# Kernel tuning notes

Hardware: AMD Instinct MI355X
Metric: run time of the kernel (lower is better)

The kernel has to match this reference:

```python
import jax, jax.numpy as jnp
import numpy as np

B, S, D_MODEL, N_HEADS, HEAD_DIM = 4, 2048, 1024, 16, 64
NEG = -1e9


def apply_rope_real(x, cos_f, sin_f):
    # x: [B, H, S, D]; cos_f/sin_f: [S, D//2] broadcast over B, H
    x_even = x[..., ::2]
    x_odd = x[..., 1::2]
    out_even = x_even * cos_f - x_odd * sin_f
    out_odd = x_even * sin_f + x_odd * cos_f
    return jnp.stack([out_even, out_odd], axis=-1).reshape(x.shape)


def setup_inputs() -> dict:
    key = jax.random.key(0)
    ks = jax.random.split(key, 8)
    x = jax.random.normal(ks[0], (B, S, D_MODEL), dtype=jnp.float32)
    # RoPE tables: theta_i = 10000^{-2i/d}, angles = pos * theta
    inv_freq = 1.0 / (10000.0 ** (jnp.arange(0, HEAD_DIM, 2, dtype=jnp.float32) / HEAD_DIM))
    angles = jnp.arange(S, dtype=jnp.float32)[:, None] * inv_freq[None, :]  # [S, D/2]
    cos_freqs = jnp.cos(angles)
    sin_freqs = jnp.sin(angles)
    causal_mask = jnp.where(jnp.tril(jnp.ones((S, S), dtype=bool)), 0.0, NEG).astype(jnp.float32)
    scale = 0.02
    w_q = jax.random.normal(ks[1], (D_MODEL, D_MODEL), dtype=jnp.float32) * scale
    w_k = jax.random.normal(ks[2], (D_MODEL, D_MODEL), dtype=jnp.float32) * scale
    w_v = jax.random.normal(ks[3], (D_MODEL, D_MODEL), dtype=jnp.float32) * scale
    w_o = jax.random.normal(ks[4], (D_MODEL, D_MODEL), dtype=jnp.float32) * scale
    return {"x": x, "cos_freqs": cos_freqs, "sin_freqs": sin_freqs,
            "causal_mask": causal_mask, "w_q": w_q, "w_k": w_k, "w_v": w_v, "w_o": w_o}


def reference(x, cos_freqs, sin_freqs, causal_mask, w_q, w_k, w_v, w_o):
    batch, seq_len, _ = x.shape
    scale = 1.0 / jnp.sqrt(jnp.float32(HEAD_DIM))
    # torch Linear: y = x @ W.T
    def proj(w):
        return (x @ w.T).reshape(batch, seq_len, N_HEADS, HEAD_DIM).transpose(0, 2, 1, 3)
    q = apply_rope_real(proj(w_q), cos_freqs, sin_freqs)
    k = apply_rope_real(proj(w_k), cos_freqs, sin_freqs)
    v = proj(w_v)
    attn = jnp.einsum('bhqd,bhkd->bhqk', q, k) * scale + causal_mask
    attn = jax.nn.softmax(attn, axis=-1)
    out = jnp.einsum('bhqk,bhkd->bhqd', attn, v)
    out = out.transpose(0, 2, 1, 3).reshape(batch, seq_len, -1)
    return out @ w_o.T
```

## Files before the change

kernel.cpp:

```cpp
#include <hip/hip_runtime.h>
#include <stdint.h>

#define B_  4
#define S_  2048
#define DM_ 1024
#define NH_ 16
#define HD_ 64

typedef unsigned short ushort_t;
typedef __bf16 bf16x8 __attribute__((ext_vector_type(8)));
typedef float  floatx4 __attribute__((ext_vector_type(4)));
typedef float  floatx16 __attribute__((ext_vector_type(16)));

__device__ __forceinline__ float bf2f(ushort_t u) {
    union { unsigned int i; float f; } v; v.i = ((unsigned int)u) << 16; return v.f;
}
__device__ __forceinline__ ushort_t f2bf(float f) {
    union { float f; unsigned int i; } v; v.f = f;
    unsigned int x = v.i;
    return (ushort_t)((x + 0x7fffu + ((x >> 16) & 1u)) >> 16);
}
__device__ __forceinline__ unsigned int pack_bf16_trunc(float lo, float hi) {
    union { float f; unsigned int u; } a, b;
    a.f = lo; b.f = hi;
    return __builtin_amdgcn_perm(b.u, a.u, 0x07060302u);
}

__global__ __launch_bounds__(256) void cvt_all_kernel(
    const float* __restrict__ x,  const float* __restrict__ wq,
    const float* __restrict__ wk, const float* __restrict__ wv,
    const float* __restrict__ wo,
    ushort_t* __restrict__ xb,  ushort_t* __restrict__ wqb,
    ushort_t* __restrict__ wkb, ushort_t* __restrict__ wvb,
    ushort_t* __restrict__ wob)
{
    const int blk = blockIdx.x;
    const float* src; ushort_t* dst; int off;
    if (blk < 8192)       { src = x;  dst = xb;  off = blk; }
    else if (blk < 9216)  { src = wq; dst = wqb; off = blk - 8192; }
    else if (blk < 10240) { src = wk; dst = wkb; off = blk - 9216; }
    else if (blk < 11264) { src = wv; dst = wvb; off = blk - 10240; }
    else                  { src = wo; dst = wob; off = blk - 11264; }
    const int i = off * 256 + threadIdx.x;
    float4 v = ((const float4*)src)[i];
    ushort4 o; o.x = f2bf(v.x); o.y = f2bf(v.y); o.z = f2bf(v.z); o.w = f2bf(v.w);
    ((ushort4*)dst)[i] = o;
}

__global__ __launch_bounds__(256) void gemm_bt_kernel(
    const ushort_t* __restrict__ A,
    const ushort_t* __restrict__ B0, const ushort_t* __restrict__ B1,
    const ushort_t* __restrict__ B2,
    void* __restrict__ C0, void* __restrict__ C1, void* __restrict__ C2,
    int M, int N, int K, int mode)
{
    __shared__ ushort_t As[128 * 64];
    __shared__ ushort_t Bs[128 * 64];
    const int z = blockIdx.z;
    const ushort_t* Bw = z == 0 ? B0 : z == 1 ? B1 : B2;
    void* Cv           = z == 0 ? C0 : z == 1 ? C1 : C2;

    const int tid  = threadIdx.x;
    const int mbase = blockIdx.x * 128;
    const int nbase = blockIdx.y * 128;
    const int wave = tid >> 6, lane = tid & 63;
    const int l15 = lane & 15, quad = lane >> 4;
    const int wm = (wave & 1) * 64, wn = (wave >> 1) * 64;

    floatx4 acc[4][4] = {};

    for (int kt = 0; kt < K; kt += 64) {
        __syncthreads();
#pragma unroll
        for (int r = 0; r < 4; ++r) {
            const int e   = tid * 8 + r * 2048;
            const int kk  = e >> 12;
            const int row = (e >> 5) & 127;
            const int c   = e & 31;
            const ushort_t* ga = A  + (size_t)(mbase + row) * K + kt + kk * 32 + c;
            const ushort_t* gb = Bw + (size_t)(nbase + row) * K + kt + kk * 32 + c;
            __builtin_amdgcn_global_load_lds(
                (const __attribute__((address_space(1))) unsigned int*)ga,
                (__attribute__((address_space(3))) unsigned int*)(As + e), 16, 0, 0);
            __builtin_amdgcn_global_load_lds(
                (const __attribute__((address_space(1))) unsigned int*)gb,
                (__attribute__((address_space(3))) unsigned int*)(Bs + e), 16, 0, 0);
        }
        __builtin_amdgcn_s_waitcnt(0);
        __syncthreads();

#pragma unroll
        for (int kk = 0; kk < 2; ++kk) {
            bf16x8 af[4], bfr[4];
#pragma unroll
            for (int t = 0; t < 4; ++t) {
                af[t]  = *(const bf16x8*)(As + kk * 4096 + (wm + t * 16 + l15) * 32 + quad * 8);
                bfr[t] = *(const bf16x8*)(Bs + kk * 4096 + (wn + t * 16 + l15) * 32 + quad * 8);
            }
#pragma unroll
            for (int mt = 0; mt < 4; ++mt)
#pragma unroll
                for (int nt = 0; nt < 4; ++nt)
                    acc[mt][nt] = __builtin_amdgcn_mfma_f32_16x16x32_bf16(
                        af[mt], bfr[nt], acc[mt][nt], 0, 0, 0);
        }
    }

    const bool vtmode = (mode == 0) && (z == 2);
#pragma unroll
    for (int mt = 0; mt < 4; ++mt) {
#pragma unroll
        for (int nt = 0; nt < 4; ++nt) {
            const int col = nbase + wn + nt * 16 + l15;
            const int m0  = mbase + wm + mt * 16 + quad * 4;
            if (vtmode) {
                const int b = m0 >> 11, s = m0 & 2047;
                const int hh = col >> 6, d = col & 63;
                uint2 pk;
                pk.x = (unsigned)f2bf(acc[mt][nt][0]) | ((unsigned)f2bf(acc[mt][nt][1]) << 16);
                pk.y = (unsigned)f2bf(acc[mt][nt][2]) | ((unsigned)f2bf(acc[mt][nt][3]) << 16);
                *(uint2*)&((ushort_t*)Cv)[((size_t)((b * NH_ + hh) * HD_ + d)) * S_ + s] = pk;
            } else if (mode == 0) {
#pragma unroll
                for (int r = 0; r < 4; ++r) {
                    const int m = m0 + r;
                    const int b = m >> 11, s = m & 2047;
                    const int hh = col >> 6, d = col & 63;
                    ((ushort_t*)Cv)[(((size_t)(b * NH_ + hh)) * S_ + s) * HD_ + d] =
                        f2bf(acc[mt][nt][r]);
                }
            } else {
#pragma unroll
                for (int r = 0; r < 4; ++r)
                    ((float*)Cv)[(size_t)(m0 + r) * N + col] = acc[mt][nt][r];
            }
        }
    }
}

#define QSCALE 0.1803368801f
__global__ __launch_bounds__(256) void rope_kernel(
    ushort_t* __restrict__ q, ushort_t* __restrict__ k,
    const float* __restrict__ cf, const float* __restrict__ sf)
{
    const int idx = blockIdx.x * 256 + threadIdx.x;
    const int j = idx & 31;
    const int s = (idx >> 5) & (S_ - 1);
    const float c  = cf[s * 32 + j];
    const float sn = sf[s * 32 + j];
    const size_t base = (size_t)idx * 2;
    float qe = bf2f(q[base]), qo = bf2f(q[base + 1]);
    q[base]     = f2bf((qe * c - qo * sn) * QSCALE);
    q[base + 1] = f2bf((qe * sn + qo * c) * QSCALE);
    float ke = bf2f(k[base]), ko = bf2f(k[base + 1]);
    k[base]     = f2bf(ke * c - ko * sn);
    k[base + 1] = f2bf(ke * sn + ko * c);
}

__global__ __launch_bounds__(256, 2) void attn_kernel(
    const ushort_t* __restrict__ Qg, const ushort_t* __restrict__ Kg,
    const ushort_t* __restrict__ Vg, ushort_t* __restrict__ Og)
{
    __shared__ ushort_t Ks[64 * 72];
    __shared__ ushort_t Vt[64 * 72];
    __shared__ ushort_t Pt[4][32 * 64];

    const int pair = blockIdx.x;
    const int bh   = blockIdx.y;
    const int tid  = threadIdx.x;
    const int wave = tid >> 6, lane = tid & 63;
    const int l31 = lane & 31, h = lane >> 5;

    const size_t bh_off = (size_t)bh * S_ * HD_;
    const int trow = tid >> 3;
    const int tcol = (tid & 7) * 8;
    const int pswz = (l31 & 7) << 3;
    const int b_out = bh >> 4, h_out = bh & 15;

#pragma unroll 1
    for (int seg = 0; seg < 2; ++seg) {
        const int qtile = seg ? (15 - pair) : pair;
        const int qbase = qtile * 128;
        const int nkt   = 2 * qtile + 2;
        const int qrow  = qbase + wave * 32 + l31;

        bf16x8 qf[4];
#pragma unroll
        for (int ks = 0; ks < 4; ++ks)
            qf[ks] = *(const bf16x8*)(Qg + bh_off + (size_t)qrow * HD_ + ks * 16 + h * 8);

        float m_run = -1e30f, l_run = 0.f;
        floatx16 o_acc[2] = {};

        for (int kt = 0; kt < nkt; ++kt) {
            const int kbase = kt * 64;
            __syncthreads();
#pragma unroll
            for (int r = 0; r < 2; ++r) {
                const int row = trow + r * 32;
                *(bf16x8*)(Ks + row * 72 + tcol) =
                    *(const bf16x8*)(Kg + bh_off + (size_t)(kbase + row) * HD_ + tcol);
                const int c = tid + r * 256;
                const int d = c >> 3, k0 = (c & 7) * 8;
                bf16x8 vv = *(const bf16x8*)(Vg + bh_off + (size_t)d * S_ + kbase + k0);
                *(bf16x8*)(Vt + d * 72 + (k0 ^ (((d >> 3) & 7) << 3))) = vv;
            }
            __syncthreads();

            if (kbase > qbase + wave * 32 + 31) continue;

            floatx16 st[2] = {};
#pragma unroll
            for (int nt = 0; nt < 2; ++nt) {
                const ushort_t* kr = Ks + (nt * 32 + l31) * 72 + h * 8;
#pragma unroll
                for (int ks = 0; ks < 4; ++ks) {
                    bf16x8 kf = *(const bf16x8*)(kr + ks * 16);
                    st[nt] = __builtin_amdgcn_mfma_f32_32x32x16_bf16(kf, qf[ks], st[nt], 0, 0, 0);
                }
            }
            if (kbase + 63 > qbase + wave * 32) {
#pragma unroll
                for (int nt = 0; nt < 2; ++nt) {
                    const int key0 = kbase + nt * 32 + 4 * h;
#pragma unroll
                    for (int c = 0; c < 4; ++c)
#pragma unroll
                        for (int r = 0; r < 4; ++r)
                            if (key0 + 8 * c + r > qrow) st[nt][c * 4 + r] = -1e9f;
                }
            }
            float mx = st[0][0];
#pragma unroll
            for (int nt = 0; nt < 2; ++nt)
#pragma unroll
                for (int i = 0; i < 16; ++i) mx = fmaxf(mx, st[nt][i]);
            mx = fmaxf(mx, __shfl_xor(mx, 32, 64));
            const float mnew = fmaxf(m_run, mx);
            const float alpha = __builtin_amdgcn_exp2f(m_run - mnew);
            m_run = mnew;
            float sum = 0.f;
#pragma unroll
            for (int nt = 0; nt < 2; ++nt)
#pragma unroll
                for (int i = 0; i < 16; ++i) {
                    const float p = __builtin_amdgcn_exp2f(st[nt][i] - mnew);
                    st[nt][i] = p; sum += p;
                }
            sum += __shfl_xor(sum, 32, 64);
            l_run = l_run * alpha + sum;
#pragma unroll
            for (int dt = 0; dt < 2; ++dt)
#pragma unroll
                for (int i = 0; i < 16; ++i) o_acc[dt][i] *= alpha;

            ushort_t* pr = &Pt[wave][l31 * 64];
#pragma unroll
            for (int nt = 0; nt < 2; ++nt)
#pragma unroll
                for (int c = 0; c < 4; ++c) {
                    uint2 pk;
                    pk.x = pack_bf16_trunc(st[nt][c * 4 + 0], st[nt][c * 4 + 1]);
                    pk.y = pack_bf16_trunc(st[nt][c * 4 + 2], st[nt][c * 4 + 3]);
                    *(uint2*)(pr + (((nt * 32 + 8 * c) ^ pswz) + 4 * h)) = pk;
                }
            __builtin_amdgcn_fence(__ATOMIC_ACQ_REL, "wavefront");
            __builtin_amdgcn_wave_barrier();

            bf16x8 pf[4];
#pragma unroll
            for (int ks = 0; ks < 4; ++ks)
                pf[ks] = *(const bf16x8*)(&Pt[wave][l31 * 64 + ((ks * 16 + h * 8) ^ pswz)]);

#pragma unroll
            for (int dt = 0; dt < 2; ++dt) {
                const int d = dt * 32 + l31;
                const int sw = ((d >> 3) & 7) << 3;
                const ushort_t* vr = Vt + d * 72;
#pragma unroll
                for (int ks = 0; ks < 4; ++ks) {
                    bf16x8 vf = *(const bf16x8*)(vr + ((ks * 16 + h * 8) ^ sw));
                    o_acc[dt] = __builtin_amdgcn_mfma_f32_32x32x16_bf16(vf, pf[ks], o_acc[dt], 0, 0, 0);
                }
            }
        }

        const float inv = 1.0f / l_run;
        ushort_t* orow = Og + ((size_t)(b_out * S_ + qrow)) * DM_ + h_out * HD_;
#pragma unroll
        for (int dt = 0; dt < 2; ++dt)
#pragma unroll
            for (int c = 0; c < 4; ++c) {
                uint2 pk;
                pk.x = (unsigned)f2bf(o_acc[dt][c * 4 + 0] * inv) |
                       ((unsigned)f2bf(o_acc[dt][c * 4 + 1] * inv) << 16);
                pk.y = (unsigned)f2bf(o_acc[dt][c * 4 + 2] * inv) |
                       ((unsigned)f2bf(o_acc[dt][c * 4 + 3] * inv) << 16);
                *(uint2*)(orow + dt * 32 + 8 * c + 4 * h) = pk;
            }
    }
}

extern "C" void kernel_launch(void* const* d_in, const int* in_sizes, int n_in,
                              void* d_out, int out_size, void* d_ws, size_t ws_size,
                              hipStream_t stream)
{
    const float* x  = (const float*)d_in[0];
    const float* cf = (const float*)d_in[1];
    const float* sf = (const float*)d_in[2];
    const float* wq = (const float*)d_in[4];
    const float* wk = (const float*)d_in[5];
    const float* wv = (const float*)d_in[6];
    const float* wo = (const float*)d_in[7];
    float* out = (float*)d_out;

    const size_t NELEM = (size_t)B_ * S_ * DM_;
    const size_t WELEM = (size_t)DM_ * DM_;
    ushort_t* xb  = (ushort_t*)d_ws;
    ushort_t* qb  = xb + NELEM;
    ushort_t* kb  = qb + NELEM;
    ushort_t* vb  = kb + NELEM;
    ushort_t* ao  = vb + NELEM;
    ushort_t* wqb = ao + NELEM;
    ushort_t* wkb = wqb + WELEM;
    ushort_t* wvb = wkb + WELEM;
    ushort_t* wob = wvb + WELEM;

    cvt_all_kernel<<<dim3(8192 + 4 * 1024), 256, 0, stream>>>(
        x, wq, wk, wv, wo, xb, wqb, wkb, wvb, wob);

    const int M = B_ * S_;
    gemm_bt_kernel<<<dim3(M / 128, DM_ / 128, 3), 256, 0, stream>>>(
        xb, wqb, wkb, wvb, qb, kb, vb, M, DM_, DM_, 0);
    rope_kernel<<<dim3((B_ * NH_ * S_ * 32) / 256), 256, 0, stream>>>(qb, kb, cf, sf);
    attn_kernel<<<dim3(8, B_ * NH_), 256, 0, stream>>>(qb, kb, vb, ao);
    gemm_bt_kernel<<<dim3(M / 128, DM_ / 128, 1), 256, 0, stream>>>(
        ao, wob, wob, wob, out, out, out, M, DM_, DM_, 1);
}
```

Baseline: 284.3 us.

## Rewrite GEMM as 256x256 double-buffered pipeline with swizzled LDS and 8 waves

The projection GEMM now uses 256x256 block tiles with 512 threads, double-buffered LDS holding full 64-wide K tiles, and an XOR swizzle on LDS chunks to avoid bank conflicts. Loads for the next A tile and the B tile two steps ahead are issued between four MFMA quadrants, with fine-grained barriers and s_setprio so memory traffic overlaps compute. This is meant to raise data reuse and hide global-load latency. In exchange the kernel holds a larger accumulator array per wave and uses 128KB of LDS. The grid also shrinks, which may underfill the CUs on the output projection.

```diff
diff --git a/kernel.cpp b/kernel.cpp
--- a/kernel.cpp
+++ b/kernel.cpp
@@ -47,72 +47,167 @@
     ((ushort4*)dst)[i] = o;
 }
 
-__global__ __launch_bounds__(256) void gemm_bt_kernel(
+__global__ __launch_bounds__(512, 2) void gemm_bt_kernel(
     const ushort_t* __restrict__ A,
     const ushort_t* __restrict__ B0, const ushort_t* __restrict__ B1,
     const ushort_t* __restrict__ B2,
     void* __restrict__ C0, void* __restrict__ C1, void* __restrict__ C2,
     int M, int N, int K, int mode)
 {
-    __shared__ ushort_t As[128 * 64];
-    __shared__ ushort_t Bs[128 * 64];
+    __shared__ ushort_t As[2][16384];
+    __shared__ ushort_t Bs[2][16384];
+
     const int z = blockIdx.z;
     const ushort_t* Bw = z == 0 ? B0 : z == 1 ? B1 : B2;
     void* Cv           = z == 0 ? C0 : z == 1 ? C1 : C2;
 
     const int tid  = threadIdx.x;
-    const int mbase = blockIdx.x * 128;
-    const int nbase = blockIdx.y * 128;
     const int wave = tid >> 6, lane = tid & 63;
     const int l15 = lane & 15, quad = lane >> 4;
-    const int wm = (wave & 1) * 64, wn = (wave >> 1) * 64;
-
-    floatx4 acc[4][4] = {};
-
-    for (int kt = 0; kt < K; kt += 64) {
-        __syncthreads();
-#pragma unroll
-        for (int r = 0; r < 4; ++r) {
-            const int e   = tid * 8 + r * 2048;
-            const int kk  = e >> 12;
-            const int row = (e >> 5) & 127;
-            const int c   = e & 31;
-            const ushort_t* ga = A  + (size_t)(mbase + row) * K + kt + kk * 32 + c;
-            const ushort_t* gb = Bw + (size_t)(nbase + row) * K + kt + kk * 32 + c;
+    const int wr = wave >> 2, wc = wave & 3;
+    const int mbase = blockIdx.x * 256;
+    const int nbase = blockIdx.y * 256;
+    const int NT = K >> 6;
+
+    const int srow = lane >> 3;
+    const int schk = (lane & 7) ^ srow;
+
+    auto stageA = [&](int b, int t, int h) {
+#pragma unroll
+        for (int j = 0; j < 2; ++j) {
+            const int idx = wave * 2 + j;
+            const int r = h * 128 + idx * 8 + srow;
+            const ushort_t* src = A + (size_t)(mbase + r) * K + t * 64 + schk * 8;
             __builtin_amdgcn_global_load_lds(
-                (const __attribute__((address_space(1))) unsigned int*)ga,
-                (__attribute__((address_space(3))) unsigned int*)(As + e), 16, 0, 0);
+                (const __attribute__((address_space(1))) unsigned int*)src,
+                (__attribute__((address_space(3))) unsigned int*)(&As[b][h * 8192 + idx * 512 + lane * 8]),
+                16, 0, 0);
+        }
+    };
+    auto stageB = [&](int b, int t, int h) {
+#pragma unroll
+        for (int j = 0; j < 2; ++j) {
+            const int idx = wave * 2 + j;
+            const int r = h * 128 + idx * 8 + srow;
+            const ushort_t* src = Bw + (size_t)(nbase + r) * K + t * 64 + schk * 8;
             __builtin_amdgcn_global_load_lds(
-                (const __attribute__((address_space(1))) unsigned int*)gb,
-                (__attribute__((address_space(3))) unsigned int*)(Bs + e), 16, 0, 0);
+                (const __attribute__((address_space(1))) unsigned int*)src,
+                (__attribute__((address_space(3))) unsigned int*)(&Bs[b][h * 8192 + idx * 512 + lane * 8]),
+                16, 0, 0);
         }
-        __builtin_amdgcn_s_waitcnt(0);
-        __syncthreads();
-
+    };
+
+    floatx4 acc[8][4] = {};
+
+    stageA(0, 0, 0); stageA(0, 0, 1);
+    stageB(0, 0, 0); stageB(0, 0, 1);
+    stageB(1, 1, 0); stageB(1, 1, 1);
+    asm volatile("s_waitcnt vmcnt(4)" ::: "memory");
+    __builtin_amdgcn_s_barrier();
+
+    auto do_tile = [&](int t, int bt) {
+        bf16x8 a0[2][4], a1[2][4], bv0[2][2], bv1[2][2];
 #pragma unroll
         for (int kk = 0; kk < 2; ++kk) {
-            bf16x8 af[4], bfr[4];
-#pragma unroll
-            for (int t = 0; t < 4; ++t) {
-                af[t]  = *(const bf16x8*)(As + kk * 4096 + (wm + t * 16 + l15) * 32 + quad * 8);
-                bfr[t] = *(const bf16x8*)(Bs + kk * 4096 + (wn + t * 16 + l15) * 32 + quad * 8);
-            }
+#pragma unroll
+            for (int f = 0; f < 4; ++f) {
+                const int row = wr * 128 + f * 16 + l15;
+                a0[kk][f] = *(const bf16x8*)&As[bt][row * 64 + (((kk << 2) | quad) ^ (l15 & 7)) * 8];
+            }
+#pragma unroll
+            for (int g = 0; g < 2; ++g) {
+                const int row = wc * 64 + g * 16 + l15;
+                bv0[kk][g] = *(const bf16x8*)&Bs[bt][row * 64 + (((kk << 2) | quad) ^ (l15 & 7)) * 8];
+            }
+        }
+        if (t + 1 < NT) stageA(bt ^ 1, t + 1, 0);
+        __builtin_amdgcn_s_barrier();
+        asm volatile("s_waitcnt lgkmcnt(0)" ::: "memory");
+        __builtin_amdgcn_s_setprio(1);
+#pragma unroll
+        for (int kk = 0; kk < 2; ++kk)
 #pragma unroll
             for (int mt = 0; mt < 4; ++mt)
 #pragma unroll
-                for (int nt = 0; nt < 4; ++nt)
+                for (int nt = 0; nt < 2; ++nt)
                     acc[mt][nt] = __builtin_amdgcn_mfma_f32_16x16x32_bf16(
-                        af[mt], bfr[nt], acc[mt][nt], 0, 0, 0);
-        }
+                        a0[kk][mt], bv0[kk][nt], acc[mt][nt], 0, 0, 0);
+        __builtin_amdgcn_s_setprio(0);
+        __builtin_amdgcn_s_barrier();
+
+#pragma unroll
+        for (int kk = 0; kk < 2; ++kk)
+#pragma unroll
+            for (int g = 0; g < 2; ++g) {
+                const int row = wc * 64 + 32 + g * 16 + l15;
+                bv1[kk][g] = *(const bf16x8*)&Bs[bt][row * 64 + (((kk << 2) | quad) ^ (l15 & 7)) * 8];
+            }
+        if (t + 1 < NT) stageA(bt ^ 1, t + 1, 1);
+        __builtin_amdgcn_s_barrier();
+        asm volatile("s_waitcnt lgkmcnt(0)" ::: "memory");
+        __builtin_amdgcn_s_setprio(1);
+#pragma unroll
+        for (int kk = 0; kk < 2; ++kk)
+#pragma unroll
+            for (int mt = 0; mt < 4; ++mt)
+#pragma unroll
+                for (int nt = 0; nt < 2; ++nt)
+                    acc[mt][2 + nt] = __builtin_amdgcn_mfma_f32_16x16x32_bf16(
+                        a0[kk][mt], bv1[kk][nt], acc[mt][2 + nt], 0, 0, 0);
+        __builtin_amdgcn_s_setprio(0);
+        __builtin_amdgcn_s_barrier();
+
+#pragma unroll
+        for (int kk = 0; kk < 2; ++kk)
+#pragma unroll
+            for (int f = 0; f < 4; ++f) {
+                const int row = wr * 128 + 64 + f * 16 + l15;
+                a1[kk][f] = *(const bf16x8*)&As[bt][row * 64 + (((kk << 2) | quad) ^ (l15 & 7)) * 8];
+            }
+        if (t + 2 < NT) stageB(bt, t + 2, 0);
+        __builtin_amdgcn_s_barrier();
+        asm volatile("s_waitcnt lgkmcnt(0)" ::: "memory");
+        __builtin_amdgcn_s_setprio(1);
+#pragma unroll
+        for (int kk = 0; kk < 2; ++kk)
+#pragma unroll
+            for (int mt = 0; mt < 4; ++mt)
+#pragma unroll
+                for (int nt = 0; nt < 2; ++nt)
+                    acc[4 + mt][2 + nt] = __builtin_amdgcn_mfma_f32_16x16x32_bf16(
+                        a1[kk][mt], bv1[kk][nt], acc[4 + mt][2 + nt], 0, 0, 0);
+        __builtin_amdgcn_s_setprio(0);
+        __builtin_amdgcn_s_barrier();
+
+        if (t + 2 < NT) stageB(bt, t + 2, 1);
+        __builtin_amdgcn_s_barrier();
+        __builtin_amdgcn_s_setprio(1);
+#pragma unroll
+        for (int kk = 0; kk < 2; ++kk)
+#pragma unroll
+            for (int mt = 0; mt < 4; ++mt)
+#pragma unroll
+                for (int nt = 0; nt < 2; ++nt)
+                    acc[4 + mt][nt] = __builtin_amdgcn_mfma_f32_16x16x32_bf16(
+                        a1[kk][mt], bv0[kk][nt], acc[4 + mt][nt], 0, 0, 0);
+        __builtin_amdgcn_s_setprio(0);
+        if (t < NT - 2) { asm volatile("s_waitcnt vmcnt(4)" ::: "memory"); }
+        else            { asm volatile("s_waitcnt vmcnt(0)" ::: "memory"); }
+        __builtin_amdgcn_s_barrier();
+    };
+
+    for (int t = 0; t < NT; t += 2) {
+        do_tile(t, 0);
+        do_tile(t + 1, 1);
     }
 
     const bool vtmode = (mode == 0) && (z == 2);
 #pragma unroll
-    for (int mt = 0; mt < 4; ++mt) {
+    for (int mt = 0; mt < 8; ++mt) {
 #pragma unroll
         for (int nt = 0; nt < 4; ++nt) {
-            const int col = nbase + wn + nt * 16 + l15;
-            const int m0  = mbase + wm + mt * 16 + quad * 4;
+            const int col = nbase + wc * 64 + nt * 16 + l15;
+            const int m0  = mbase + wr * 128 + mt * 16 + quad * 4;
             if (vtmode) {
                 const int b = m0 >> 11, s = m0 & 2047;
                 const int hh = col >> 6, d = col & 63;
@@ -330,10 +425,10 @@
         x, wq, wk, wv, wo, xb, wqb, wkb, wvb, wob);
 
     const int M = B_ * S_;
-    gemm_bt_kernel<<<dim3(M / 128, DM_ / 128, 3), 256, 0, stream>>>(
+    gemm_bt_kernel<<<dim3(M / 256, DM_ / 256, 3), 512, 0, stream>>>(
         xb, wqb, wkb, wvb, qb, kb, vb, M, DM_, DM_, 0);
     rope_kernel<<<dim3((B_ * NH_ * S_ * 32) / 256), 256, 0, stream>>>(qb, kb, cf, sf);
     attn_kernel<<<dim3(8, B_ * NH_), 256, 0, stream>>>(qb, kb, vb, ao);
-    gemm_bt_kernel<<<dim3(M / 128, DM_ / 128, 1), 256, 0, stream>>>(
+    gemm_bt_kernel<<<dim3(M / 256, DM_ / 256, 1), 512, 0, stream>>>(
         ao, wob, wob, wob, out, out, out, M, DM_, DM_, 1);
 }
```

After: 287.3 us. About the same (+1.1%).
